# Kernel optimization log

Measured on AMD Instinct MI355X. Metric: run time of the kernel, lower is better.

Reference implementation:

```python
import jax, jax.numpy as jnp
import numpy as np

KERNEL_MUL = 2.0
KERNEL_NUM = 5


def setup_inputs() -> dict:
    key = jax.random.key(0)
    k1, k2 = jax.random.split(key)
    N, D = 4096, 256
    source = jax.random.normal(k1, (N, D), dtype=jnp.float32)
    target = jax.random.normal(k2, (N, D), dtype=jnp.float32)
    return {"source": source, "target": target}


def reference(source, target):
    ns = source.shape[0]
    total = jnp.concatenate([source, target], axis=0)  # [2N, D]
    n = total.shape[0]
    # Pairwise squared L2 distance via GEMM trick (same math as expand+sub+square+sum)
    sq = jnp.sum(total * total, axis=1)               # [2N]
    gram = total @ total.T                             # [2N, 2N]
    l2 = sq[:, None] + sq[None, :] - 2.0 * gram        # [2N, 2N]
    # Bandwidth from detached distances (torch uses .data)
    l2_sg = jax.lax.stop_gradient(l2)
    bandwidth = jnp.sum(l2_sg) / (n * n - n)
    bandwidth = bandwidth / (KERNEL_MUL ** (KERNEL_NUM // 2))
    bws = bandwidth * (KERNEL_MUL ** jnp.arange(KERNEL_NUM, dtype=l2.dtype))  # [K]
    # Multi-kernel Gaussian RBF sum: sum_k exp(-l2 / bw_k)
    kernels = jnp.exp(-l2[None, :, :] / bws[:, None, None]).sum(axis=0)  # [2N, 2N]
    XX = kernels[:ns, :ns]
    YY = kernels[ns:, ns:]
    XY = kernels[:ns, ns:]
    YX = kernels[ns:, :ns]
    loss = jnp.mean(XX) + jnp.mean(YY) - jnp.mean(XY) - jnp.mean(YX)
    return loss
```

## Files before the change

kernel.cpp:

```cpp
#include <hip/hip_runtime.h>
#include <hip/hip_bf16.h>
#include <stdint.h>


#define NROW 8192
#define NS   4096
#define DD   256
#define TILE 128
#define BK   64
#define NTB  64
#define NBLK (NTB*(NTB+1)/2)
#define K1B  128

typedef __bf16 bf16_t;
typedef __bf16 bf16x8 __attribute__((ext_vector_type(8)));
typedef __bf16 bf16x4 __attribute__((ext_vector_type(4)));
typedef float  f32x4  __attribute__((ext_vector_type(4)));

#define OFF_CPAR 0
#define OFF_SQ   1024
#define OFF_CS   (OFF_SQ + 8192*4)
#define OFF_SS   (OFF_CS + K1B*256*4)
#define OFF_PART (OFF_SS + 1024)
#define OFF_TBF  (1<<18)

__device__ __forceinline__ void async16(const void* g, void* l) {
  __builtin_amdgcn_global_load_lds(
      (const __attribute__((address_space(1))) void*)(uintptr_t)g,
      (__attribute__((address_space(3))) void*)(uintptr_t)l, 16, 0, 0);
}

__global__ __launch_bounds__(256) void k1_prep(const float* __restrict__ src,
                                               const float* __restrict__ tgt,
                                               float* __restrict__ sq,
                                               float* __restrict__ cs_part,
                                               float* __restrict__ ss_part,
                                               bf16_t* __restrict__ tbf) {
  const int b = blockIdx.x, tid = threadIdx.x;
  const int w = tid >> 6, lane = tid & 63;
  float4 csum = make_float4(0.f, 0.f, 0.f, 0.f);
  float wss = 0.f;
  for (int r = 0; r < 16; ++r) {
    const int row = b * 64 + w * 16 + r;
    const float* rp = (row < NS) ? (src + (size_t)row * DD)
                                 : (tgt + (size_t)(row - NS) * DD);
    float4 v = ((const float4*)rp)[lane];
    bf16x4 o;
    o[0] = (bf16_t)v.x; o[1] = (bf16_t)v.y; o[2] = (bf16_t)v.z; o[3] = (bf16_t)v.w;
    *(bf16x4*)(tbf + (size_t)row * DD + lane * 4) = o;
    float s2 = v.x*v.x + v.y*v.y + v.z*v.z + v.w*v.w;
    #pragma unroll
    for (int off = 32; off >= 1; off >>= 1) s2 += __shfl_xor(s2, off);
    if (lane == 0) { sq[row] = s2; wss += s2; }
    csum.x += v.x; csum.y += v.y; csum.z += v.z; csum.w += v.w;
  }
  __shared__ float cls[4][256];
  __shared__ float sls[4];
  ((float4*)cls[w])[lane] = csum;
  if (lane == 0) sls[w] = wss;
  __syncthreads();
  cs_part[b * 256 + tid] = cls[0][tid] + cls[1][tid] + cls[2][tid] + cls[3][tid];
  if (tid == 0) ss_part[b] = sls[0] + sls[1] + sls[2] + sls[3];
}

__global__ __launch_bounds__(256) void k2_bw(const float* __restrict__ cs_part,
                                             const float* __restrict__ ss_part,
                                             float* __restrict__ cpar) {
  const int tid = threadIdx.x, w = tid >> 6, lane = tid & 63;
  float c = 0.f;
  for (int b = 0; b < K1B; ++b) c += cs_part[b * 256 + tid];
  double csq = (double)c * (double)c;
  double ssq = (tid < K1B) ? (double)ss_part[tid] : 0.0;
  #pragma unroll
  for (int off = 32; off >= 1; off >>= 1) {
    csq += __shfl_xor(csq, off);
    ssq += __shfl_xor(ssq, off);
  }
  __shared__ double rc[4], rs[4];
  if (lane == 0) { rc[w] = csq; rs[w] = ssq; }
  __syncthreads();
  if (tid == 0) {
    double C = rc[0] + rc[1] + rc[2] + rc[3];
    double S = rs[0] + rs[1] + rs[2] + rs[3];
    const double n = (double)NROW;
    double suml2 = 2.0 * n * S - 2.0 * C;
    double bw0 = suml2 / (n * n - n) / 4.0;
    cpar[0] = (float)(1.4426950408889634 / (16.0 * bw0));
  }
}

__global__ __launch_bounds__(256) void k3_mmd(const bf16_t* __restrict__ tbf,
                                              const float* __restrict__ sqg,
                                              const float* __restrict__ cpar,
                                              float* __restrict__ part) {
  __shared__ __align__(16) bf16_t As[TILE * BK];
  __shared__ __align__(16) bf16_t Bs[TILE * BK];
  __shared__ float red[4];

  const int t = blockIdx.x;
  int bi = (int)((sqrtf(8.0f * (float)t + 1.0f) - 1.0f) * 0.5f);
  while ((bi + 1) * (bi + 2) / 2 <= t) ++bi;
  while (bi * (bi + 1) / 2 > t) --bi;
  const int bj = t - bi * (bi + 1) / 2;

  const int tid = threadIdx.x;
  const int w = tid >> 6, lane = tid & 63;
  const int m0 = (w >> 1) * 64, n0 = (w & 1) * 64;
  const int wbase = tid & ~63;

  const float cE = cpar[0];

  f32x4 acc[4][4] = {};

  const bf16_t* Ag = tbf + (size_t)bi * TILE * DD;
  const bf16_t* Bg = tbf + (size_t)bj * TILE * DD;

  for (int kt = 0; kt < 4; ++kt) {
    __syncthreads();
    #pragma unroll
    for (int it = 0; it < 4; ++it) {
      const int c  = it * 256 + tid;
      const int r  = c >> 3;
      const int kk = (c & 7) * 8;
      char* ldst = (char*)As + (size_t)(it * 256 + wbase) * 16;
      async16(Ag + (size_t)r * DD + kt * 64 + kk, ldst);
      char* ldst2 = (char*)Bs + (size_t)(it * 256 + wbase) * 16;
      async16(Bg + (size_t)r * DD + kt * 64 + kk, ldst2);
    }
    __syncthreads();
    #pragma unroll
    for (int kk = 0; kk < 2; ++kk) {
      bf16x8 af[4], bfr[4];
      #pragma unroll
      for (int mi = 0; mi < 4; ++mi)
        af[mi] = *(const bf16x8*)(As + (m0 + mi * 16 + (lane & 15)) * BK +
                                  kk * 32 + (lane >> 4) * 8);
      #pragma unroll
      for (int ni = 0; ni < 4; ++ni)
        bfr[ni] = *(const bf16x8*)(Bs + (n0 + ni * 16 + (lane & 15)) * BK +
                                   kk * 32 + (lane >> 4) * 8);
      #pragma unroll
      for (int mi = 0; mi < 4; ++mi)
        #pragma unroll
        for (int ni = 0; ni < 4; ++ni)
          acc[mi][ni] = __builtin_amdgcn_mfma_f32_16x16x32_bf16(
              af[mi], bfr[ni], acc[mi][ni], 0, 0, 0);
    }
  }

  const float c2 = 2.0f * cE;
  float bjv[4];
  #pragma unroll
  for (int ni = 0; ni < 4; ++ni)
    bjv[ni] = sqg[bj * TILE + n0 + ni * 16 + (lane & 15)] * cE;

  float tsum = 0.f;
  #pragma unroll
  for (int mi = 0; mi < 4; ++mi) {
    float ai[4];
    #pragma unroll
    for (int r = 0; r < 4; ++r)
      ai[r] = sqg[bi * TILE + m0 + mi * 16 + (lane >> 4) * 4 + r] * cE;
    #pragma unroll
    for (int ni = 0; ni < 4; ++ni) {
      #pragma unroll
      for (int r = 0; r < 4; ++r) {
        const float g = acc[mi][ni][r];
        const float e = fmaf(g, c2, -(ai[r] + bjv[ni]));
        const float v   = __builtin_amdgcn_exp2f(e);
        const float v2  = v * v;
        const float v4  = v2 * v2;
        const float v8  = v4 * v4;
        const float v16 = v8 * v8;
        tsum += v + v2 + v4 + v8 + v16;
      }
    }
  }
  #pragma unroll
  for (int off = 32; off >= 1; off >>= 1) tsum += __shfl_xor(tsum, off);
  if (lane == 0) red[w] = tsum;
  __syncthreads();
  if (tid == 0) {
    const float s    = red[0] + red[1] + red[2] + red[3];
    const float sign = ((bi < NS / TILE) == (bj < NS / TILE)) ? 1.f : -1.f;
    const float wt   = (bi == bj) ? 1.f : 2.f;
    part[t] = s * sign * wt;
  }
}

__global__ __launch_bounds__(256) void k4_fin(const float* __restrict__ part,
                                              float* __restrict__ out) {
  const int tid = threadIdx.x, w = tid >> 6, lane = tid & 63;
  double s = 0.0;
  for (int i = tid; i < NBLK; i += 256) s += (double)part[i];
  #pragma unroll
  for (int off = 32; off >= 1; off >>= 1) s += __shfl_xor(s, off);
  __shared__ double rd[4];
  if (lane == 0) rd[w] = s;
  __syncthreads();
  if (tid == 0)
    out[0] = (float)((rd[0] + rd[1] + rd[2] + rd[3]) /
                     ((double)NS * (double)NS));
}

extern "C" void kernel_launch(void* const* d_in, const int* in_sizes, int n_in,
                              void* d_out, int out_size, void* d_ws, size_t ws_size,
                              hipStream_t stream) {
  const float* src = (const float*)d_in[0];
  const float* tgt = (const float*)d_in[1];
  char* ws = (char*)d_ws;
  float*  cpar = (float*)(ws + OFF_CPAR);
  float*  sq   = (float*)(ws + OFF_SQ);
  float*  csp  = (float*)(ws + OFF_CS);
  float*  ssp  = (float*)(ws + OFF_SS);
  float*  part = (float*)(ws + OFF_PART);
  bf16_t* tbf  = (bf16_t*)(ws + OFF_TBF);

  k1_prep<<<K1B, 256, 0, stream>>>(src, tgt, sq, csp, ssp, tbf);
  k2_bw  <<<1,   256, 0, stream>>>(csp, ssp, cpar);
  k3_mmd <<<NBLK,256, 0, stream>>>(tbf, sq, cpar, part);
  k4_fin <<<1,   256, 0, stream>>>(part, (float*)d_out);
}
```

Before: 108.1 us.

## Swizzle LDS tiles to avoid bank conflicts and fuse final reduction via atomics

Applies an XOR swizzle to the LDS chunk placement of the A/B tiles so the MFMA fragment reads across rows spread over banks instead of conflicting. It also drops the final reduction kernel: each tile block atomically adds its scaled partial into the output, which is zeroed in the prep kernel. This saves a launch and a pass over partials, but makes accumulation order nondeterministic and float rather than double precision.

```diff
diff --git a/kernel.cpp b/kernel.cpp
--- a/kernel.cpp
+++ b/kernel.cpp
@@ -21,7 +21,6 @@
 #define OFF_SQ   1024
 #define OFF_CS   (OFF_SQ + 8192*4)
 #define OFF_SS   (OFF_CS + K1B*256*4)
-#define OFF_PART (OFF_SS + 1024)
 #define OFF_TBF  (1<<18)
 
 __device__ __forceinline__ void async16(const void* g, void* l) {
@@ -35,9 +34,11 @@
                                                float* __restrict__ sq,
                                                float* __restrict__ cs_part,
                                                float* __restrict__ ss_part,
-                                               bf16_t* __restrict__ tbf) {
+                                               bf16_t* __restrict__ tbf,
+                                               float* __restrict__ out) {
   const int b = blockIdx.x, tid = threadIdx.x;
   const int w = tid >> 6, lane = tid & 63;
+  if (b == 0 && tid == 0) out[0] = 0.f;
   float4 csum = make_float4(0.f, 0.f, 0.f, 0.f);
   float wss = 0.f;
   for (int r = 0; r < 16; ++r) {
@@ -92,7 +93,7 @@
 __global__ __launch_bounds__(256) void k3_mmd(const bf16_t* __restrict__ tbf,
                                               const float* __restrict__ sqg,
                                               const float* __restrict__ cpar,
-                                              float* __restrict__ part) {
+                                              float* __restrict__ out) {
   __shared__ __align__(16) bf16_t As[TILE * BK];
   __shared__ __align__(16) bf16_t Bs[TILE * BK];
   __shared__ float red[4];
@@ -119,26 +120,28 @@
     __syncthreads();
     #pragma unroll
     for (int it = 0; it < 4; ++it) {
-      const int c  = it * 256 + tid;
-      const int r  = c >> 3;
-      const int kk = (c & 7) * 8;
-      char* ldst = (char*)As + (size_t)(it * 256 + wbase) * 16;
-      async16(Ag + (size_t)r * DD + kt * 64 + kk, ldst);
+      const int c   = it * 256 + tid;
+      const int r   = c >> 3;
+      const int kcs = (c & 7) ^ (r & 7);
+      const bf16_t* asrc = Ag + (size_t)r * DD + kt * 64 + kcs * 8;
+      const bf16_t* bsrc = Bg + (size_t)r * DD + kt * 64 + kcs * 8;
+      char* ldst  = (char*)As + (size_t)(it * 256 + wbase) * 16;
       char* ldst2 = (char*)Bs + (size_t)(it * 256 + wbase) * 16;
-      async16(Bg + (size_t)r * DD + kt * 64 + kk, ldst2);
+      async16(asrc, ldst);
+      async16(bsrc, ldst2);
     }
     __syncthreads();
     #pragma unroll
     for (int kk = 0; kk < 2; ++kk) {
+      const int kc = kk * 4 + (lane >> 4);
+      const int kphys = (kc ^ (lane & 7)) * 8;
       bf16x8 af[4], bfr[4];
       #pragma unroll
       for (int mi = 0; mi < 4; ++mi)
-        af[mi] = *(const bf16x8*)(As + (m0 + mi * 16 + (lane & 15)) * BK +
-                                  kk * 32 + (lane >> 4) * 8);
+        af[mi] = *(const bf16x8*)(As + (m0 + mi * 16 + (lane & 15)) * BK + kphys);
       #pragma unroll
       for (int ni = 0; ni < 4; ++ni)
-        bfr[ni] = *(const bf16x8*)(Bs + (n0 + ni * 16 + (lane & 15)) * BK +
-                                   kk * 32 + (lane >> 4) * 8);
+        bfr[ni] = *(const bf16x8*)(Bs + (n0 + ni * 16 + (lane & 15)) * BK + kphys);
       #pragma unroll
       for (int mi = 0; mi < 4; ++mi)
         #pragma unroll
@@ -184,23 +187,8 @@
     const float s    = red[0] + red[1] + red[2] + red[3];
     const float sign = ((bi < NS / TILE) == (bj < NS / TILE)) ? 1.f : -1.f;
     const float wt   = (bi == bj) ? 1.f : 2.f;
-    part[t] = s * sign * wt;
-  }
-}
-
-__global__ __launch_bounds__(256) void k4_fin(const float* __restrict__ part,
-                                              float* __restrict__ out) {
-  const int tid = threadIdx.x, w = tid >> 6, lane = tid & 63;
-  double s = 0.0;
-  for (int i = tid; i < NBLK; i += 256) s += (double)part[i];
-  #pragma unroll
-  for (int off = 32; off >= 1; off >>= 1) s += __shfl_xor(s, off);
-  __shared__ double rd[4];
-  if (lane == 0) rd[w] = s;
-  __syncthreads();
-  if (tid == 0)
-    out[0] = (float)((rd[0] + rd[1] + rd[2] + rd[3]) /
-                     ((double)NS * (double)NS));
+    atomicAdd(out, s * sign * wt * (1.0f / ((float)NS * (float)NS)));
+  }
 }
 
 extern "C" void kernel_launch(void* const* d_in, const int* in_sizes, int n_in,
@@ -213,11 +201,10 @@
   float*  sq   = (float*)(ws + OFF_SQ);
   float*  csp  = (float*)(ws + OFF_CS);
   float*  ssp  = (float*)(ws + OFF_SS);
-  float*  part = (float*)(ws + OFF_PART);
   bf16_t* tbf  = (bf16_t*)(ws + OFF_TBF);
-
-  k1_prep<<<K1B, 256, 0, stream>>>(src, tgt, sq, csp, ssp, tbf);
+  float*  out  = (float*)d_out;
+
+  k1_prep<<<K1B, 256, 0, stream>>>(src, tgt, sq, csp, ssp, tbf, out);
   k2_bw  <<<1,   256, 0, stream>>>(csp, ssp, cpar);
-  k3_mmd <<<NBLK,256, 0, stream>>>(tbf, sq, cpar, part);
-  k4_fin <<<1,   256, 0, stream>>>(part, (float*)d_out);
-}
+  k3_mmd <<<NBLK,256, 0, stream>>>(tbf, sq, cpar, out);
+}
```

After: 110.3 us. 2.1% more time.
